# Optimization experiments

Measured on AMD Instinct MI355X. Metric: run time of the kernel, lower is better.

The kernel has to match this reference:

```python
import jax, jax.numpy as jnp
import numpy as np

EMB_DIM = 2048
NUM_HEADS = 16
HEAD_DIM = EMB_DIM // NUM_HEADS  # 128
B, T = 4, 2048


def setup_inputs() -> dict:
    key = jax.random.key(0)
    ks = jax.random.split(key, 6)
    s = lambda fan_in: 1.0 / np.sqrt(fan_in)
    return {
        "x": jax.random.normal(ks[0], (B, T, EMB_DIM), dtype=jnp.float32),
        # weights stored [in, out] so forward is x @ W
        "Wq": jax.random.normal(ks[1], (EMB_DIM, EMB_DIM), dtype=jnp.float32) * s(EMB_DIM),
        "Wk": jax.random.normal(ks[2], (EMB_DIM, HEAD_DIM), dtype=jnp.float32) * s(EMB_DIM),
        "Wv": jax.random.normal(ks[3], (EMB_DIM, HEAD_DIM), dtype=jnp.float32) * s(EMB_DIM),
        "Wo": jax.random.normal(ks[4], (EMB_DIM, EMB_DIM), dtype=jnp.float32) * s(EMB_DIM),
        "bo": jax.random.normal(ks[5], (EMB_DIM,), dtype=jnp.float32) * 0.01,
    }


def reference(x, Wq, Wk, Wv, Wo, bo):
    Bsz, Tlen, C = x.shape
    H, D = NUM_HEADS, HEAD_DIM
    q = (x @ Wq).reshape(Bsz, Tlen, H, D)          # [B,T,H,D]
    k = x @ Wk                                      # [B,T,D] (single shared head)
    v = x @ Wv                                      # [B,T,D]
    # MQA: K/V broadcast over heads via einsum (no expand materialization)
    scores = jnp.einsum("bihd,bjd->bhij", q, k) / jnp.sqrt(jnp.float32(D))
    i = jnp.arange(Tlen)[:, None]
    j = jnp.arange(Tlen)[None, :]
    causal = j <= i                                  # attend to past & self
    scores = jnp.where(causal, scores, -jnp.inf)
    attn = jax.nn.softmax(scores, axis=-1)           # [B,H,T,T]
    out = jnp.einsum("bhij,bjd->bihd", attn, v).reshape(Bsz, Tlen, C)
    return out @ Wo + bo
```

## Files before the change

### kernel.cpp

```cpp
#include <hip/hip_runtime.h>
#include <stdint.h>

typedef __attribute__((ext_vector_type(8))) short short8;
typedef __attribute__((ext_vector_type(4))) float floatx4;

#define TLEN 2048
#define BATCH 4
#define EMB 2048
#define NHEADS 16
#define HDIM 128
#define MROWS (BATCH * TLEN)
#define QTILES (TLEN / 64)

struct TrueT  { static constexpr bool value = true;  };
struct FalseT { static constexpr bool value = false; };

__device__ __forceinline__ ushort f2bf(float f) {
    union { float f; uint32_t u; } v; v.f = f;
    uint32_t u = v.u;
    return (ushort)((u + 0x7fffu + ((u >> 16) & 1u)) >> 16);
}

__device__ __forceinline__ uint32_t cvt_pk_bf16(float a, float b) {
    uint32_t r;
    asm volatile("v_cvt_pk_bf16_f32 %0, %1, %2" : "=v"(r) : "v"(a), "v"(b));
    return r;
}

__device__ __forceinline__ void async_copy16(const ushort* g, ushort* l) {
    __builtin_amdgcn_global_load_lds(
        (const __attribute__((address_space(1))) uint32_t*)g,
        (__attribute__((address_space(3))) uint32_t*)l, 16, 0, 0);
}

__global__ __launch_bounds__(256) void cast_bf16_kernel(const float* __restrict__ in,
                                                        ushort* __restrict__ out, int n) {
    int i = (blockIdx.x * 256 + threadIdx.x) * 4;
    if (i >= n) return;
    float4 f = *(const float4*)(in + i);
    ushort4 o;
    o.x = f2bf(f.x); o.y = f2bf(f.y); o.z = f2bf(f.z); o.w = f2bf(f.w);
    *(ushort4*)(out + i) = o;
}

__global__ void transpose_cast_kernel(const float* __restrict__ in, ushort* __restrict__ out,
                                      int R, int Cc) {
    __shared__ float tile[32][33];
    int x = blockIdx.x * 32 + threadIdx.x;
    int y0 = blockIdx.y * 32;
#pragma unroll
    for (int i = 0; i < 4; i++) {
        int y = y0 + threadIdx.y + i * 8;
        tile[threadIdx.y + i * 8][threadIdx.x] = in[(size_t)y * Cc + x];
    }
    __syncthreads();
    int xo = y0 + threadIdx.x;
#pragma unroll
    for (int i = 0; i < 4; i++) {
        int yo = blockIdx.x * 32 + threadIdx.y + i * 8;
        out[(size_t)yo * R + xo] = f2bf(tile[threadIdx.x][threadIdx.y + i * 8]);
    }
}

template <int MODE>
__global__ __launch_bounds__(256) void gemm_bt_kernel(const ushort* __restrict__ A,
                                                      const ushort* __restrict__ Bt,
                                                      void* __restrict__ Cp,
                                                      void* __restrict__ Cp2,
                                                      const float* __restrict__ bias,
                                                      int M, int N, int K) {
    __shared__ ushort As[128 * 64];
    __shared__ ushort Bs[128 * 64];
    int tid = threadIdx.x;
    int wid = tid >> 6, lane = tid & 63;
    int quad = lane >> 4, l15 = lane & 15;
    int m0 = blockIdx.y * 128;
    int n0 = blockIdx.x * 128;
    int rm = (wid >> 1) * 64;
    int cn = (wid & 1) * 64;
    int grow = lane >> 3;
    int gcol = (lane & 7) * 8;

    floatx4 acc[4][4];
#pragma unroll
    for (int i = 0; i < 4; i++)
#pragma unroll
        for (int j = 0; j < 4; j++)
#pragma unroll
            for (int r = 0; r < 4; r++) acc[i][j][r] = 0.f;

    for (int kk = 0; kk < K; kk += 64) {
#pragma unroll
        for (int c = 0; c < 4; c++) {
            int chunk = wid * 4 + c;
            int row = chunk * 8 + grow;
            async_copy16(A + (size_t)(m0 + row) * K + kk + gcol, &As[chunk * 512]);
            async_copy16(Bt + (size_t)(n0 + row) * K + kk + gcol, &Bs[chunk * 512]);
        }
        __syncthreads();
#pragma unroll
        for (int ks = 0; ks < 64; ks += 32) {
            short8 af[4], bf[4];
#pragma unroll
            for (int i = 0; i < 4; i++)
                af[i] = *(const short8*)(&As[(rm + i * 16 + l15) * 64 + ks + quad * 8]);
#pragma unroll
            for (int j = 0; j < 4; j++)
                bf[j] = *(const short8*)(&Bs[(cn + j * 16 + l15) * 64 + ks + quad * 8]);
#pragma unroll
            for (int i = 0; i < 4; i++)
#pragma unroll
                for (int j = 0; j < 4; j++)
                    acc[i][j] = __builtin_amdgcn_mfma_f32_16x16x32_bf16(af[i], bf[j], acc[i][j], 0, 0, 0);
        }
        __syncthreads();
    }
#pragma unroll
    for (int i = 0; i < 4; i++)
#pragma unroll
        for (int j = 0; j < 4; j++) {
            if (MODE == 2 && n0 != 0) {
                int d = cn + j * 16 + l15;
                int row = m0 + rm + i * 16 + quad * 4;
                ushort4 o;
                o.x = f2bf(acc[i][j][0]); o.y = f2bf(acc[i][j][1]);
                o.z = f2bf(acc[i][j][2]); o.w = f2bf(acc[i][j][3]);
                *(ushort4*)((ushort*)Cp2 + (size_t)d * M + row) = o;
            } else {
#pragma unroll
                for (int r = 0; r < 4; r++) {
                    int row = m0 + rm + i * 16 + quad * 4 + r;
                    int col = n0 + cn + j * 16 + l15;
                    float v = acc[i][j][r];
                    if (MODE == 0) {
                        ((ushort*)Cp)[(size_t)row * N + col] = f2bf(v);
                    } else if (MODE == 1) {
                        ((float*)Cp)[(size_t)row * N + col] = v + bias[col];
                    } else {
                        ((ushort*)Cp)[(size_t)row * HDIM + col] = f2bf(v);
                    }
                }
            }
        }
}

__global__ __launch_bounds__(256, 2) void mqa_attn_kernel(const ushort* __restrict__ Qb,
                                                          const ushort* __restrict__ Kb,
                                                          const ushort* __restrict__ Vg,
                                                          ushort* __restrict__ Ab) {
    __shared__ ushort Ks[128 * 128];
    __shared__ ushort Vs[128 * 128];
    int tid = threadIdx.x;
    int wid = tid >> 6, lane = tid & 63;
    int quad = lane >> 4, l15 = lane & 15;
    int h0 = blockIdx.y * 2, b = blockIdx.z;
    const float scale2 = 0.08838834764831845f * 1.4426950408889634f;
    const ushort* kbase = Kb + (size_t)b * TLEN * HDIM;
    const ushort* vbase = Vg + (size_t)b * TLEN;

    int rowloc = wid * 16 + l15;
    int swz = (l15 & 7) << 3;

    auto stage = [&](int jt) {
#pragma unroll
        for (int i = 0; i < 8; i++) {
            int c = wid * 8 + i;
            int kr = c * 4 + quad;
            int kc = (l15 * 8) ^ ((kr & 7) << 3);
            async_copy16(kbase + (size_t)(jt * 128 + kr) * HDIM + kc, &Ks[c * 512]);
            int vd = c * 4 + quad;
            int vc = (l15 * 8) ^ ((vd & 7) << 3);
            async_copy16(vbase + (size_t)vd * MROWS + jt * 128 + vc, &Vs[c * 512]);
        }
    };

#pragma unroll 1
    for (int t = 0; t < 2; t++) {
        int qt = (t == 0) ? (QTILES - 1 - blockIdx.x) : blockIdx.x;
        size_t qrowbase = (size_t)b * TLEN + qt * 64;
        int dlim = rowloc + ((qt & 1) ? 64 : 0);
        bool evenqt = (qt & 1) == 0;
        int njt = qt / 2 + 1;

        short8 aq[2][4];
#pragma unroll
        for (int hh = 0; hh < 2; hh++) {
            const ushort* qp = Qb + (qrowbase + wid * 16 + l15) * EMB + (h0 + hh) * HDIM + quad * 8;
#pragma unroll
            for (int kd = 0; kd < 4; kd++) aq[hh][kd] = *(const short8*)(qp + kd * 32);
        }

        float lsum[2] = {0.f, 0.f};
        floatx4 o_acc[2][8];
#pragma unroll
        for (int hh = 0; hh < 2; hh++)
#pragma unroll
            for (int nd = 0; nd < 8; nd++)
#pragma unroll
                for (int r = 0; r < 4; r++) o_acc[hh][nd][r] = 0.f;

        auto compute_tile = [&](auto mtag) {
            constexpr bool MASKED = decltype(mtag)::value;
#pragma unroll
            for (int jp = 0; jp < 4; jp++) {
                if (MASKED && evenqt && jp >= 2) continue;
                uint32_t XA[2][2], XB[2][2];
#pragma unroll
                for (int jj = 0; jj < 2; jj++) {
                    int j = jp * 2 + jj;
                    floatx4 s0, s1;
#pragma unroll
                    for (int r = 0; r < 4; r++) { s0[r] = 0.f; s1[r] = 0.f; }
                    __builtin_amdgcn_s_setprio(1);
#pragma unroll
                    for (int kd = 0; kd < 4; kd++) {
                        short8 ak = *(const short8*)(&Ks[(j * 16 + l15) * 128 + ((kd * 32 + quad * 8) ^ swz)]);
                        s0 = __builtin_amdgcn_mfma_f32_16x16x32_bf16(ak, aq[0][kd], s0, 0, 0, 0);
                        s1 = __builtin_amdgcn_mfma_f32_16x16x32_bf16(ak, aq[1][kd], s1, 0, 0, 0);
                    }
                    __builtin_amdgcn_s_setprio(0);
                    float e0[4], e1[4];
#pragma unroll
                    for (int r = 0; r < 4; r++) {
                        float v0 = exp2f(s0[r] * scale2);
                        float v1 = exp2f(s1[r] * scale2);
                        if constexpr (MASKED) {
                            int key = j * 16 + quad * 4 + r;
                            if (key > dlim) { v0 = 0.f; v1 = 0.f; }
                        }
                        e0[r] = v0; e1[r] = v1;
                        lsum[0] += v0; lsum[1] += v1;
                    }
                    XA[0][jj] = cvt_pk_bf16(e0[0], e0[1]); XB[0][jj] = cvt_pk_bf16(e0[2], e0[3]);
                    XA[1][jj] = cvt_pk_bf16(e1[0], e1[1]); XB[1][jj] = cvt_pk_bf16(e1[2], e1[3]);
                }
                short8 pf[2];
#pragma unroll
                for (int hh = 0; hh < 2; hh++) {
                    uint32_t xA = XA[hh][0], yA = XA[hh][1];
                    uint32_t xB = XB[hh][0], yB = XB[hh][1];
                    asm volatile("v_permlane32_swap_b32 %0, %1" : "+v"(xA), "+v"(yA));
                    asm volatile("v_permlane16_swap_b32 %0, %1" : "+v"(xA), "+v"(yA));
                    asm volatile("v_permlane32_swap_b32 %0, %1" : "+v"(xB), "+v"(yB));
                    asm volatile("v_permlane16_swap_b32 %0, %1" : "+v"(xB), "+v"(yB));
                    union { uint32_t u[4]; short8 s; } fu;
                    fu.u[0] = xA; fu.u[1] = xB; fu.u[2] = yA; fu.u[3] = yB;
                    pf[hh] = fu.s;
                }
                __builtin_amdgcn_s_setprio(1);
#pragma unroll
                for (int nd = 0; nd < 8; nd++) {
                    short8 vf = *(const short8*)(&Vs[(nd * 16 + l15) * 128 + ((jp * 32 + quad * 8) ^ swz)]);
                    o_acc[0][nd] = __builtin_amdgcn_mfma_f32_16x16x32_bf16(pf[0], vf, o_acc[0][nd], 0, 0, 0);
                    o_acc[1][nd] = __builtin_amdgcn_mfma_f32_16x16x32_bf16(pf[1], vf, o_acc[1][nd], 0, 0, 0);
                }
                __builtin_amdgcn_s_setprio(0);
            }
        };

#pragma unroll 1
        for (int jt = 0; jt < njt - 1; ++jt) {
            stage(jt);
            __syncthreads();
            compute_tile(FalseT{});
            __syncthreads();
        }
        {
            stage(njt - 1);
            __syncthreads();
            compute_tile(TrueT{});
            __syncthreads();
        }

#pragma unroll
        for (int hh = 0; hh < 2; hh++) {
            float ls = lsum[hh];
            ls += __shfl_xor(ls, 16);
            ls += __shfl_xor(ls, 32);
            float inv_l[4];
#pragma unroll
            for (int r = 0; r < 4; r++) inv_l[r] = 1.f / __shfl(ls, quad * 4 + r, 16);
#pragma unroll
            for (int nd = 0; nd < 8; nd++)
#pragma unroll
                for (int r = 0; r < 4; r++) {
                    size_t row = qrowbase + wid * 16 + quad * 4 + r;
                    int col = (h0 + hh) * HDIM + nd * 16 + l15;
                    Ab[row * EMB + col] = f2bf(o_acc[hh][nd][r] * inv_l[r]);
                }
        }
    }
}

extern "C" void kernel_launch(void* const* d_in, const int* in_sizes, int n_in,
                              void* d_out, int out_size, void* d_ws, size_t ws_size,
                              hipStream_t stream) {
    const float* x  = (const float*)d_in[0];
    const float* Wq = (const float*)d_in[1];
    const float* Wk = (const float*)d_in[2];
    const float* Wv = (const float*)d_in[3];
    const float* Wo = (const float*)d_in[4];
    const float* bo = (const float*)d_in[5];
    float* out = (float*)d_out;

    ushort* ws = (ushort*)d_ws;
    ushort* Xb    = ws;
    ushort* Wq_t  = Xb    + (size_t)MROWS * EMB;
    ushort* Wkv_t = Wq_t  + (size_t)EMB * EMB;
    ushort* Wo_t  = Wkv_t + (size_t)256 * EMB;
    ushort* Qb    = Wo_t  + (size_t)EMB * EMB;
    ushort* Kb    = Qb    + (size_t)MROWS * EMB;
    ushort* Vg    = Kb    + (size_t)MROWS * HDIM;
    ushort* Ab    = Vg    + (size_t)HDIM * MROWS;

    cast_bf16_kernel<<<dim3(MROWS * EMB / 1024), 256, 0, stream>>>(x, Xb, MROWS * EMB);
    transpose_cast_kernel<<<dim3(EMB / 32, EMB / 32), dim3(32, 8), 0, stream>>>(Wq, Wq_t, EMB, EMB);
    transpose_cast_kernel<<<dim3(HDIM / 32, EMB / 32), dim3(32, 8), 0, stream>>>(Wk, Wkv_t, EMB, HDIM);
    transpose_cast_kernel<<<dim3(HDIM / 32, EMB / 32), dim3(32, 8), 0, stream>>>(Wv, Wkv_t + (size_t)HDIM * EMB, EMB, HDIM);
    transpose_cast_kernel<<<dim3(EMB / 32, EMB / 32), dim3(32, 8), 0, stream>>>(Wo, Wo_t, EMB, EMB);

    gemm_bt_kernel<0><<<dim3(EMB / 128, MROWS / 128), 256, 0, stream>>>(Xb, Wq_t, Qb, nullptr, nullptr, MROWS, EMB, EMB);
    gemm_bt_kernel<2><<<dim3(2, MROWS / 128), 256, 0, stream>>>(Xb, Wkv_t, Kb, Vg, nullptr, MROWS, 256, EMB);
    mqa_attn_kernel<<<dim3(QTILES / 2, NHEADS / 2, BATCH), 256, 0, stream>>>(Qb, Kb, Vg, Ab);
    gemm_bt_kernel<1><<<dim3(EMB / 128, MROWS / 128), 256, 0, stream>>>(Ab, Wo_t, out, nullptr, bo, MROWS, EMB, EMB);
}
```

Baseline: 477.4 us.

## Use 256x256-tile triple-buffered GEMM kernel for Q and output projections

Adds a new GEMM kernel with 256x256 output tiles, 512 threads, a three-stage async-copy LDS pipeline with swizzled layout, and MFMA priority hints. The Q projection and the output projection now use it instead of the 128x128 kernel. Larger tiles raise arithmetic intensity and cut global loads per FLOP. The cost is fewer blocks (256 per GEMM), heavier register pressure from 128 accumulators per thread, and more LDS per block, which may limit occupancy or leave the 256 CUs unevenly loaded.

Result: no change. 468.3 us (-1.9%).

```diff
diff --git a/kernel.cpp b/kernel.cpp
--- a/kernel.cpp
+++ b/kernel.cpp
@@ -144,6 +144,100 @@
         }
 }
 
+template <int MODE>
+__global__ __launch_bounds__(512, 2) void gemm256_kernel(const ushort* __restrict__ A,
+                                                         const ushort* __restrict__ Bt,
+                                                         void* __restrict__ Cp,
+                                                         const float* __restrict__ bias,
+                                                         int M, int N, int K) {
+    __shared__ ushort As[3][256 * 32];
+    __shared__ ushort Bs[3][256 * 32];
+    int tid = threadIdx.x;
+    int wid = tid >> 6, lane = tid & 63;
+    int quad = lane >> 4, l15 = lane & 15;
+    int wr = wid >> 2, wc = wid & 3;
+    int m0 = blockIdx.y * 256, n0 = blockIdx.x * 256;
+
+    int srow = lane >> 2;
+    int scol = (((lane & 3) ^ ((lane >> 2) & 3) ^ ((lane >> 4) & 3))) * 8;
+    int rdsw = (quad ^ ((l15 ^ (l15 >> 2)) & 3)) * 8;
+
+    floatx4 acc[8][4];
+#pragma unroll
+    for (int m = 0; m < 8; m++)
+#pragma unroll
+        for (int n = 0; n < 4; n++)
+#pragma unroll
+            for (int r = 0; r < 4; r++) acc[m][n][r] = 0.f;
+
+    auto stage = [&](int t) {
+        int slot = t % 3;
+        int kk = t * 32;
+#pragma unroll
+        for (int i = 0; i < 2; i++) {
+            int c = wid * 2 + i;
+            int row = c * 16 + srow;
+            async_copy16(A + (size_t)(m0 + row) * K + kk + scol, &As[slot][c * 512]);
+            async_copy16(Bt + (size_t)(n0 + row) * K + kk + scol, &Bs[slot][c * 512]);
+        }
+    };
+
+    auto compute = [&](int t) {
+        int slot = t % 3;
+        const ushort* as = &As[slot][0];
+        const ushort* bs = &Bs[slot][0];
+        short8 af[8], bf[4];
+#pragma unroll
+        for (int m = 0; m < 8; m++)
+            af[m] = *(const short8*)(&as[(wr * 128 + m * 16 + l15) * 32 + rdsw]);
+#pragma unroll
+        for (int n = 0; n < 4; n++)
+            bf[n] = *(const short8*)(&bs[(wc * 64 + n * 16 + l15) * 32 + rdsw]);
+        __builtin_amdgcn_s_setprio(1);
+#pragma unroll
+        for (int m = 0; m < 8; m++)
+#pragma unroll
+            for (int n = 0; n < 4; n++)
+                acc[m][n] = __builtin_amdgcn_mfma_f32_16x16x32_bf16(af[m], bf[n], acc[m][n], 0, 0, 0);
+        __builtin_amdgcn_s_setprio(0);
+    };
+
+    int NT = K >> 5;
+
+    stage(0);
+    stage(1);
+    asm volatile("s_waitcnt vmcnt(4)" ::: "memory");
+    __builtin_amdgcn_s_barrier();
+
+#pragma unroll 1
+    for (int t = 0; t < NT - 2; ++t) {
+        stage(t + 2);
+        compute(t);
+        asm volatile("s_waitcnt vmcnt(4)" ::: "memory");
+        __builtin_amdgcn_s_barrier();
+    }
+    compute(NT - 2);
+    asm volatile("s_waitcnt vmcnt(0)" ::: "memory");
+    __builtin_amdgcn_s_barrier();
+    compute(NT - 1);
+
+#pragma unroll
+    for (int m = 0; m < 8; m++)
+#pragma unroll
+        for (int n = 0; n < 4; n++)
+#pragma unroll
+            for (int r = 0; r < 4; r++) {
+                int row = m0 + wr * 128 + m * 16 + quad * 4 + r;
+                int col = n0 + wc * 64 + n * 16 + l15;
+                float v = acc[m][n][r];
+                if (MODE == 0) {
+                    ((ushort*)Cp)[(size_t)row * N + col] = f2bf(v);
+                } else {
+                    ((float*)Cp)[(size_t)row * N + col] = v + bias[col];
+                }
+            }
+}
+
 __global__ __launch_bounds__(256, 2) void mqa_attn_kernel(const ushort* __restrict__ Qb,
                                                           const ushort* __restrict__ Kb,
                                                           const ushort* __restrict__ Vg,
@@ -319,8 +413,8 @@
     transpose_cast_kernel<<<dim3(HDIM / 32, EMB / 32), dim3(32, 8), 0, stream>>>(Wv, Wkv_t + (size_t)HDIM * EMB, EMB, HDIM);
     transpose_cast_kernel<<<dim3(EMB / 32, EMB / 32), dim3(32, 8), 0, stream>>>(Wo, Wo_t, EMB, EMB);
 
-    gemm_bt_kernel<0><<<dim3(EMB / 128, MROWS / 128), 256, 0, stream>>>(Xb, Wq_t, Qb, nullptr, nullptr, MROWS, EMB, EMB);
+    gemm256_kernel<0><<<dim3(EMB / 256, MROWS / 256), 512, 0, stream>>>(Xb, Wq_t, Qb, nullptr, MROWS, EMB, EMB);
     gemm_bt_kernel<2><<<dim3(2, MROWS / 128), 256, 0, stream>>>(Xb, Wkv_t, Kb, Vg, nullptr, MROWS, 256, EMB);
     mqa_attn_kernel<<<dim3(QTILES / 2, NHEADS / 2, BATCH), 256, 0, stream>>>(Qb, Kb, Vg, Ab);
-    gemm_bt_kernel<1><<<dim3(EMB / 128, MROWS / 128), 256, 0, stream>>>(Ab, Wo_t, out, nullptr, bo, MROWS, EMB, EMB);
-}
+    gemm256_kernel<1><<<dim3(EMB / 256, MROWS / 256), 512, 0, stream>>>(Ab, Wo_t, out, bo, MROWS, EMB, EMB);
+}
```
